# Optimization experiments

Measured on AMD Instinct MI355X. Metric: run time of the kernel, lower is better.

Reference implementation:

```python
import jax, jax.numpy as jnp
import numpy as np
from jax import lax

GUARD_CELLS = 80
BG_CELLS = 80
ALPHA = 1.8
CFAR_UNITS = 1 + 2 * GUARD_CELLS + 2 * BG_CELLS          # 321
GUARD_UNITS = 2 * GUARD_CELLS + 1                         # 161
BG_AREA = CFAR_UNITS ** 2 - GUARD_UNITS ** 2              # background ring cell count
FRONT_DIV = (GUARD_UNITS ** 2) * ALPHA


def box_sum(x, k):
    """Same-padded KxK box sum over NCHW x (C=1), via separable 1D convs.

    Mathematically identical to a Conv2d with all-ones KxK kernel, zero bias,
    padding (k-1)//2 -- but O(N*K) instead of O(N*K^2).
    """
    p = (k - 1) // 2
    kh = jnp.ones((1, 1, k, 1), x.dtype)  # OIHW
    kw = jnp.ones((1, 1, 1, k), x.dtype)
    y = lax.conv_general_dilated(x, kh, window_strides=(1, 1), padding=[(p, p), (0, 0)])
    y = lax.conv_general_dilated(y, kw, window_strides=(1, 1), padding=[(0, 0), (p, p)])
    return y


def setup_inputs() -> dict:
    key = jax.random.key(0)
    x = jax.random.uniform(key, (4, 1, 1024, 1024), dtype=jnp.float32)
    return {"x": x}


def reference(x) -> jnp.ndarray:
    allsum = box_sum(x, CFAR_UNITS)            # conv1: 321x321 ones box
    front = box_sum(x, GUARD_UNITS)            # conv2: 161x161 ones box
    back = (allsum - front) / jnp.float32(BG_AREA)     # div1: 1x1 conv = scale
    front = front / jnp.float32(FRONT_DIV)             # div2: 1x1 conv = scale
    return front / back
```

## Files before the change

### kernel.cpp

```cpp
#include <hip/hip_runtime.h>
#include <hip/hip_bf16.h>


#define IMG 4
#define H 1024
#define W 1024
#define NSEG 32
#define SEGR 32
#define PADL 164
#define PADR 164
#define ROWLEN (PADL + W + PADR)

__global__ __launch_bounds__(256) void hbox_kernel(const float* __restrict__ x,
                                                   float* __restrict__ h161,
                                                   float* __restrict__ h321) {
    __shared__ float P[4][ROWLEN];
    const int wave = threadIdx.x >> 6;
    const int lane = threadIdx.x & 63;
    const int row  = (blockIdx.x << 2) + wave;

    const float4* xr = reinterpret_cast<const float4*>(x + (size_t)row * W);
    float v[16];
    {
        float4 a0 = xr[(lane << 2) + 0];
        float4 a1 = xr[(lane << 2) + 1];
        float4 a2 = xr[(lane << 2) + 2];
        float4 a3 = xr[(lane << 2) + 3];
        v[0]=a0.x; v[1]=a0.y; v[2]=a0.z; v[3]=a0.w;
        v[4]=a1.x; v[5]=a1.y; v[6]=a1.z; v[7]=a1.w;
        v[8]=a2.x; v[9]=a2.y; v[10]=a2.z; v[11]=a2.w;
        v[12]=a3.x; v[13]=a3.y; v[14]=a3.z; v[15]=a3.w;
    }
    float s = 0.f;
#pragma unroll
    for (int j = 0; j < 16; ++j) { s += v[j]; v[j] = s; }
    float t = s;
#pragma unroll
    for (int d = 1; d < 64; d <<= 1) {
        float u = __shfl_up(t, d, 64);
        if (lane >= d) t += u;
    }
    const float off = t - s;
#pragma unroll
    for (int j = 0; j < 16; ++j) v[j] += off;
    const float tot = __shfl(t, 63, 64);

    float* rowP = P[wave];
    float4* Pr = reinterpret_cast<float4*>(rowP + PADL);
    Pr[(lane << 2) + 0] = make_float4(v[0], v[1], v[2], v[3]);
    Pr[(lane << 2) + 1] = make_float4(v[4], v[5], v[6], v[7]);
    Pr[(lane << 2) + 2] = make_float4(v[8], v[9], v[10], v[11]);
    Pr[(lane << 2) + 3] = make_float4(v[12], v[13], v[14], v[15]);
    {
        float4* Pz = reinterpret_cast<float4*>(rowP);
        if (lane < 41) {
            Pz[lane]       = make_float4(0.f, 0.f, 0.f, 0.f);
            Pz[297 + lane] = make_float4(tot, tot, tot, tot);
        }
    }
    __syncthreads();

    const float* Pw = &P[wave][PADL];
    float* o161 = h161 + (size_t)row * W;
    float* o321 = h321 + (size_t)row * W;
#pragma unroll
    for (int k = 0; k < 16; ++k) {
        const int c = lane + (k << 6);
        const float s1 = Pw[c + 80]  - Pw[c - 81];
        const float s3 = Pw[c + 160] - Pw[c - 161];
        o161[c] = s1;
        o321[c] = s3;
    }
}

__global__ __launch_bounds__(256) void vscan_kernel(float* __restrict__ h161,
                                                    float* __restrict__ h321,
                                                    float* __restrict__ Btot) {
    const int img = blockIdx.x >> 5;
    const int seg = blockIdx.x & 31;
    const int q   = threadIdx.x;
    const int r0  = seg << 5;

    float* buf = blockIdx.y ? h321 : h161;
    float4* p = reinterpret_cast<float4*>(buf + ((size_t)img << 20) + ((size_t)r0 << 10)) + q;

    float ax = 0.f, ay = 0.f, az = 0.f, aw = 0.f;
#pragma unroll
    for (int jj = 0; jj < SEGR; jj += 8) {
        float4 a[8];
#pragma unroll
        for (int j = 0; j < 8; ++j) a[j] = p[(size_t)(jj + j) << 8];
#pragma unroll
        for (int j = 0; j < 8; ++j) {
            ax += a[j].x; ay += a[j].y; az += a[j].z; aw += a[j].w;
            a[j] = make_float4(ax, ay, az, aw);
        }
#pragma unroll
        for (int j = 0; j < 8; ++j) p[(size_t)(jj + j) << 8] = a[j];
    }
    float4* bt = reinterpret_cast<float4*>(
        Btot + ((((size_t)blockIdx.y << 2) + img) << 15) + ((size_t)seg << 10));
    bt[q] = make_float4(ax, ay, az, aw);
}

__global__ __launch_bounds__(256) void segscan_kernel(const float* __restrict__ Btot,
                                                      float* __restrict__ SP) {
    const int wid    = (blockIdx.x << 2) + (threadIdx.x >> 6);
    const int lane   = threadIdx.x & 63;
    const int bufimg = wid >> 9;
    const int pairk  = wid & 511;
    const int col    = (pairk << 1) + (lane >> 5);
    const int segl   = lane & 31;

    const size_t idx = ((size_t)bufimg << 15) + ((size_t)segl << 10) + col;
    const float v = Btot[idx];
    float t = v;
#pragma unroll
    for (int d = 1; d < 32; d <<= 1) {
        const float u = __shfl_up(t, d, 64);
        if ((lane & 31) >= d) t += u;
    }
    SP[idx] = t - v;
}

__global__ __launch_bounds__(512) void final_kernel(const float* __restrict__ g161,
                                                    const float* __restrict__ g321,
                                                    const float* __restrict__ SP,
                                                    float* __restrict__ out) {
    const int img = blockIdx.x >> 9;
    const int r   = ((blockIdx.x & 511) << 1) + (threadIdx.x >> 8);
    const int c4  = threadIdx.x & 255;

    const float4* P1 = reinterpret_cast<const float4*>(g161 + ((size_t)img << 20));
    const float4* P3 = reinterpret_cast<const float4*>(g321 + ((size_t)img << 20));
    const float4* SP1 = reinterpret_cast<const float4*>(SP) + ((size_t)img << 13);
    const float4* SP3 = reinterpret_cast<const float4*>(SP) + ((size_t)(IMG + img) << 13);

    const int hi1 = min(r + 80, H - 1),  lo1 = r - 81;
    const int hi3 = min(r + 160, H - 1), lo3 = r - 161;

    float4 f  = P1[((size_t)hi1 << 8) + c4];
    float4 fs = SP1[(((size_t)hi1 >> 5) << 8) + c4];
    float fx = f.x + fs.x, fy = f.y + fs.y, fz = f.z + fs.z, fw = f.w + fs.w;
    if (lo1 >= 0) {
        float4 g  = P1[((size_t)lo1 << 8) + c4];
        float4 gs = SP1[(((size_t)lo1 >> 5) << 8) + c4];
        fx -= g.x + gs.x; fy -= g.y + gs.y; fz -= g.z + gs.z; fw -= g.w + gs.w;
    }
    float4 a  = P3[((size_t)hi3 << 8) + c4];
    float4 as = SP3[(((size_t)hi3 >> 5) << 8) + c4];
    float ax = a.x + as.x, ay = a.y + as.y, az = a.z + as.z, aw = a.w + as.w;
    if (lo3 >= 0) {
        float4 g  = P3[((size_t)lo3 << 8) + c4];
        float4 gs = SP3[(((size_t)lo3 >> 5) << 8) + c4];
        ax -= g.x + gs.x; ay -= g.y + gs.y; az -= g.z + gs.z; aw -= g.w + gs.w;
    }

    const float SCALE = (float)(77120.0 / 46657.8);
    float4 o;
    o.x = SCALE * fx * __builtin_amdgcn_rcpf(ax - fx);
    o.y = SCALE * fy * __builtin_amdgcn_rcpf(ay - fy);
    o.z = SCALE * fz * __builtin_amdgcn_rcpf(az - fz);
    o.w = SCALE * fw * __builtin_amdgcn_rcpf(aw - fw);
    reinterpret_cast<float4*>(out + ((size_t)img << 20) + ((size_t)r << 10))[c4] = o;
}

extern "C" void kernel_launch(void* const* d_in, const int* in_sizes, int n_in,
                              void* d_out, int out_size, void* d_ws, size_t ws_size,
                              hipStream_t stream) {
    const float* x = (const float*)d_in[0];
    float* outp = (float*)d_out;
    float* h161 = (float*)d_ws;
    float* h321 = h161 + (size_t)IMG * H * W;
    float* Btot = h321 + (size_t)IMG * H * W;
    float* SPb  = Btot + (size_t)2 * IMG * NSEG * W;

    hbox_kernel<<<dim3((IMG * H) / 4), dim3(256), 0, stream>>>(x, h161, h321);
    vscan_kernel<<<dim3(128, 2), dim3(256), 0, stream>>>(h161, h321, Btot);
    segscan_kernel<<<dim3(1024), dim3(256), 0, stream>>>(Btot, SPb);
    final_kernel<<<dim3(IMG * (H / 2)), dim3(512), 0, stream>>>(h161, h321, SPb, outp);
}
```

Before: 96.03 us.

## Fuse horizontal box sum with segmented vertical scan in one kernel

Merges the horizontal box-sum kernel and the vertical segment-scan kernel. Each block now takes 8 rows, computes the horizontal 161/321 sums through shared memory, and writes vertical prefix sums within 8-row segments directly. This removes the global read-modify-write pass over both intermediate buffers. The segment count grows to 128, so the segment-scan kernel now scans 128 totals per column. It also adds extra __syncthreads per block and a larger scan-offset array.

```diff
diff --git a/kernel.cpp b/kernel.cpp
--- a/kernel.cpp
+++ b/kernel.cpp
@@ -5,122 +5,137 @@
 #define IMG 4
 #define H 1024
 #define W 1024
-#define NSEG 32
-#define SEGR 32
+#define SEGR 8
+#define NSEG 128
 #define PADL 164
 #define PADR 164
 #define ROWLEN (PADL + W + PADR)
 
-__global__ __launch_bounds__(256) void hbox_kernel(const float* __restrict__ x,
-                                                   float* __restrict__ h161,
-                                                   float* __restrict__ h321) {
+__global__ __launch_bounds__(256, 4) void hbv_kernel(const float* __restrict__ x,
+                                                     float* __restrict__ g161,
+                                                     float* __restrict__ g321,
+                                                     float* __restrict__ Btot) {
     __shared__ float P[4][ROWLEN];
+    __shared__ float Hx[4][W];
     const int wave = threadIdx.x >> 6;
     const int lane = threadIdx.x & 63;
-    const int row  = (blockIdx.x << 2) + wave;
+    const int q    = threadIdx.x;
+    const int blk  = blockIdx.x;
+    const size_t rowbase = (size_t)blk << 3;
 
-    const float4* xr = reinterpret_cast<const float4*>(x + (size_t)row * W);
-    float v[16];
-    {
-        float4 a0 = xr[(lane << 2) + 0];
-        float4 a1 = xr[(lane << 2) + 1];
-        float4 a2 = xr[(lane << 2) + 2];
-        float4 a3 = xr[(lane << 2) + 3];
-        v[0]=a0.x; v[1]=a0.y; v[2]=a0.z; v[3]=a0.w;
-        v[4]=a1.x; v[5]=a1.y; v[6]=a1.z; v[7]=a1.w;
-        v[8]=a2.x; v[9]=a2.y; v[10]=a2.z; v[11]=a2.w;
-        v[12]=a3.x; v[13]=a3.y; v[14]=a3.z; v[15]=a3.w;
+    float4 acc1 = make_float4(0.f, 0.f, 0.f, 0.f);
+    float4 acc3 = make_float4(0.f, 0.f, 0.f, 0.f);
+
+#pragma unroll
+    for (int ch = 0; ch < 2; ++ch) {
+        const size_t row = rowbase + (ch << 2) + wave;
+        {
+            const float4* xr = reinterpret_cast<const float4*>(x + row * W);
+            float v[16];
+            float4 a0 = xr[(lane << 2) + 0];
+            float4 a1 = xr[(lane << 2) + 1];
+            float4 a2 = xr[(lane << 2) + 2];
+            float4 a3 = xr[(lane << 2) + 3];
+            v[0]=a0.x; v[1]=a0.y; v[2]=a0.z; v[3]=a0.w;
+            v[4]=a1.x; v[5]=a1.y; v[6]=a1.z; v[7]=a1.w;
+            v[8]=a2.x; v[9]=a2.y; v[10]=a2.z; v[11]=a2.w;
+            v[12]=a3.x; v[13]=a3.y; v[14]=a3.z; v[15]=a3.w;
+            float s = 0.f;
+#pragma unroll
+            for (int j = 0; j < 16; ++j) { s += v[j]; v[j] = s; }
+            float t = s;
+#pragma unroll
+            for (int d = 1; d < 64; d <<= 1) {
+                float u = __shfl_up(t, d, 64);
+                if (lane >= d) t += u;
+            }
+            const float off = t - s;
+#pragma unroll
+            for (int j = 0; j < 16; ++j) v[j] += off;
+            const float tot = __shfl(t, 63, 64);
+
+            float* rowP = P[wave];
+            float4* Pr = reinterpret_cast<float4*>(rowP + PADL);
+            Pr[(lane << 2) + 0] = make_float4(v[0], v[1], v[2], v[3]);
+            Pr[(lane << 2) + 1] = make_float4(v[4], v[5], v[6], v[7]);
+            Pr[(lane << 2) + 2] = make_float4(v[8], v[9], v[10], v[11]);
+            Pr[(lane << 2) + 3] = make_float4(v[12], v[13], v[14], v[15]);
+            float4* Pz = reinterpret_cast<float4*>(rowP);
+            if (lane < 41) {
+                Pz[lane]       = make_float4(0.f, 0.f, 0.f, 0.f);
+                Pz[297 + lane] = make_float4(tot, tot, tot, tot);
+            }
+        }
+        const float* Pw = &P[wave][PADL];
+
+#pragma unroll
+        for (int k = 0; k < 16; ++k) {
+            const int c = lane + (k << 6);
+            Hx[wave][c] = Pw[c + 80] - Pw[c - 81];
+        }
+        __syncthreads();
+        {
+            float* o = g161 + (rowbase + (ch << 2)) * W;
+            const float4* Hf = reinterpret_cast<const float4*>(Hx);
+#pragma unroll
+            for (int r = 0; r < 4; ++r) {
+                float4 h = Hf[(r << 8) + q];
+                acc1.x += h.x; acc1.y += h.y; acc1.z += h.z; acc1.w += h.w;
+                reinterpret_cast<float4*>(o + (size_t)r * W)[q] = acc1;
+            }
+        }
+        __syncthreads();
+#pragma unroll
+        for (int k = 0; k < 16; ++k) {
+            const int c = lane + (k << 6);
+            Hx[wave][c] = Pw[c + 160] - Pw[c - 161];
+        }
+        __syncthreads();
+        {
+            float* o = g321 + (rowbase + (ch << 2)) * W;
+            const float4* Hf = reinterpret_cast<const float4*>(Hx);
+#pragma unroll
+            for (int r = 0; r < 4; ++r) {
+                float4 h = Hf[(r << 8) + q];
+                acc3.x += h.x; acc3.y += h.y; acc3.z += h.z; acc3.w += h.w;
+                reinterpret_cast<float4*>(o + (size_t)r * W)[q] = acc3;
+            }
+        }
+        __syncthreads();
     }
-    float s = 0.f;
-#pragma unroll
-    for (int j = 0; j < 16; ++j) { s += v[j]; v[j] = s; }
-    float t = s;
-#pragma unroll
-    for (int d = 1; d < 64; d <<= 1) {
-        float u = __shfl_up(t, d, 64);
-        if (lane >= d) t += u;
-    }
-    const float off = t - s;
-#pragma unroll
-    for (int j = 0; j < 16; ++j) v[j] += off;
-    const float tot = __shfl(t, 63, 64);
 
-    float* rowP = P[wave];
-    float4* Pr = reinterpret_cast<float4*>(rowP + PADL);
-    Pr[(lane << 2) + 0] = make_float4(v[0], v[1], v[2], v[3]);
-    Pr[(lane << 2) + 1] = make_float4(v[4], v[5], v[6], v[7]);
-    Pr[(lane << 2) + 2] = make_float4(v[8], v[9], v[10], v[11]);
-    Pr[(lane << 2) + 3] = make_float4(v[12], v[13], v[14], v[15]);
-    {
-        float4* Pz = reinterpret_cast<float4*>(rowP);
-        if (lane < 41) {
-            Pz[lane]       = make_float4(0.f, 0.f, 0.f, 0.f);
-            Pz[297 + lane] = make_float4(tot, tot, tot, tot);
-        }
-    }
-    __syncthreads();
-
-    const float* Pw = &P[wave][PADL];
-    float* o161 = h161 + (size_t)row * W;
-    float* o321 = h321 + (size_t)row * W;
-#pragma unroll
-    for (int k = 0; k < 16; ++k) {
-        const int c = lane + (k << 6);
-        const float s1 = Pw[c + 80]  - Pw[c - 81];
-        const float s3 = Pw[c + 160] - Pw[c - 161];
-        o161[c] = s1;
-        o321[c] = s3;
-    }
-}
-
-__global__ __launch_bounds__(256) void vscan_kernel(float* __restrict__ h161,
-                                                    float* __restrict__ h321,
-                                                    float* __restrict__ Btot) {
-    const int img = blockIdx.x >> 5;
-    const int seg = blockIdx.x & 31;
-    const int q   = threadIdx.x;
-    const int r0  = seg << 5;
-
-    float* buf = blockIdx.y ? h321 : h161;
-    float4* p = reinterpret_cast<float4*>(buf + ((size_t)img << 20) + ((size_t)r0 << 10)) + q;
-
-    float ax = 0.f, ay = 0.f, az = 0.f, aw = 0.f;
-#pragma unroll
-    for (int jj = 0; jj < SEGR; jj += 8) {
-        float4 a[8];
-#pragma unroll
-        for (int j = 0; j < 8; ++j) a[j] = p[(size_t)(jj + j) << 8];
-#pragma unroll
-        for (int j = 0; j < 8; ++j) {
-            ax += a[j].x; ay += a[j].y; az += a[j].z; aw += a[j].w;
-            a[j] = make_float4(ax, ay, az, aw);
-        }
-#pragma unroll
-        for (int j = 0; j < 8; ++j) p[(size_t)(jj + j) << 8] = a[j];
-    }
-    float4* bt = reinterpret_cast<float4*>(
-        Btot + ((((size_t)blockIdx.y << 2) + img) << 15) + ((size_t)seg << 10));
-    bt[q] = make_float4(ax, ay, az, aw);
+    const int img = blk >> 7;
+    const int seg = blk & 127;
+    float4* bt = reinterpret_cast<float4*>(Btot);
+    bt[((size_t)img << 15)         + (seg << 8) + q] = acc1;
+    bt[((size_t)(IMG + img) << 15) + (seg << 8) + q] = acc3;
 }
 
 __global__ __launch_bounds__(256) void segscan_kernel(const float* __restrict__ Btot,
                                                       float* __restrict__ SP) {
-    const int wid    = (blockIdx.x << 2) + (threadIdx.x >> 6);
-    const int lane   = threadIdx.x & 63;
-    const int bufimg = wid >> 9;
-    const int pairk  = wid & 511;
-    const int col    = (pairk << 1) + (lane >> 5);
-    const int segl   = lane & 31;
+    const int wid  = (blockIdx.x << 2) + (threadIdx.x >> 6);
+    const int lane = threadIdx.x & 63;
+    const int bi   = wid >> 10;
+    const int col  = wid & 1023;
+    const size_t base = ((size_t)bi << 17) + col;
 
-    const size_t idx = ((size_t)bufimg << 15) + ((size_t)segl << 10) + col;
-    const float v = Btot[idx];
-    float t = v;
+    const float a = Btot[base + ((size_t)lane << 10)];
+    const float b = Btot[base + ((size_t)(64 + lane) << 10)];
+    float t = a;
 #pragma unroll
-    for (int d = 1; d < 32; d <<= 1) {
+    for (int d = 1; d < 64; d <<= 1) {
         const float u = __shfl_up(t, d, 64);
-        if ((lane & 31) >= d) t += u;
+        if (lane >= d) t += u;
     }
-    SP[idx] = t - v;
+    const float T = __shfl(t, 63, 64);
+    float s = b;
+#pragma unroll
+    for (int d = 1; d < 64; d <<= 1) {
+        const float u = __shfl_up(s, d, 64);
+        if (lane >= d) s += u;
+    }
+    SP[base + ((size_t)lane << 10)]        = t - a;
+    SP[base + ((size_t)(64 + lane) << 10)] = T + s - b;
 }
 
 __global__ __launch_bounds__(512) void final_kernel(const float* __restrict__ g161,
@@ -133,26 +148,26 @@
 
     const float4* P1 = reinterpret_cast<const float4*>(g161 + ((size_t)img << 20));
     const float4* P3 = reinterpret_cast<const float4*>(g321 + ((size_t)img << 20));
-    const float4* SP1 = reinterpret_cast<const float4*>(SP) + ((size_t)img << 13);
-    const float4* SP3 = reinterpret_cast<const float4*>(SP) + ((size_t)(IMG + img) << 13);
+    const float4* SP1 = reinterpret_cast<const float4*>(SP) + ((size_t)img << 15);
+    const float4* SP3 = reinterpret_cast<const float4*>(SP) + ((size_t)(IMG + img) << 15);
 
     const int hi1 = min(r + 80, H - 1),  lo1 = r - 81;
     const int hi3 = min(r + 160, H - 1), lo3 = r - 161;
 
     float4 f  = P1[((size_t)hi1 << 8) + c4];
-    float4 fs = SP1[(((size_t)hi1 >> 5) << 8) + c4];
+    float4 fs = SP1[(((size_t)hi1 >> 3) << 8) + c4];
     float fx = f.x + fs.x, fy = f.y + fs.y, fz = f.z + fs.z, fw = f.w + fs.w;
     if (lo1 >= 0) {
         float4 g  = P1[((size_t)lo1 << 8) + c4];
-        float4 gs = SP1[(((size_t)lo1 >> 5) << 8) + c4];
+        float4 gs = SP1[(((size_t)lo1 >> 3) << 8) + c4];
         fx -= g.x + gs.x; fy -= g.y + gs.y; fz -= g.z + gs.z; fw -= g.w + gs.w;
     }
     float4 a  = P3[((size_t)hi3 << 8) + c4];
-    float4 as = SP3[(((size_t)hi3 >> 5) << 8) + c4];
+    float4 as = SP3[(((size_t)hi3 >> 3) << 8) + c4];
     float ax = a.x + as.x, ay = a.y + as.y, az = a.z + as.z, aw = a.w + as.w;
     if (lo3 >= 0) {
         float4 g  = P3[((size_t)lo3 << 8) + c4];
-        float4 gs = SP3[(((size_t)lo3 >> 5) << 8) + c4];
+        float4 gs = SP3[(((size_t)lo3 >> 3) << 8) + c4];
         ax -= g.x + gs.x; ay -= g.y + gs.y; az -= g.z + gs.z; aw -= g.w + gs.w;
     }
 
@@ -170,13 +185,12 @@
                               hipStream_t stream) {
     const float* x = (const float*)d_in[0];
     float* outp = (float*)d_out;
-    float* h161 = (float*)d_ws;
-    float* h321 = h161 + (size_t)IMG * H * W;
-    float* Btot = h321 + (size_t)IMG * H * W;
+    float* g161 = (float*)d_ws;
+    float* g321 = g161 + (size_t)IMG * H * W;
+    float* Btot = g321 + (size_t)IMG * H * W;
     float* SPb  = Btot + (size_t)2 * IMG * NSEG * W;
 
-    hbox_kernel<<<dim3((IMG * H) / 4), dim3(256), 0, stream>>>(x, h161, h321);
-    vscan_kernel<<<dim3(128, 2), dim3(256), 0, stream>>>(h161, h321, Btot);
-    segscan_kernel<<<dim3(1024), dim3(256), 0, stream>>>(Btot, SPb);
-    final_kernel<<<dim3(IMG * (H / 2)), dim3(512), 0, stream>>>(h161, h321, SPb, outp);
+    hbv_kernel<<<dim3(IMG * NSEG), dim3(256), 0, stream>>>(x, g161, g321, Btot);
+    segscan_kernel<<<dim3(2048), dim3(256), 0, stream>>>(Btot, SPb);
+    final_kernel<<<dim3(IMG * (H / 2)), dim3(512), 0, stream>>>(g161, g321, SPb, outp);
 }
```

After: 99.60 us. 1.04x slower.

## Fuse vertical scan, segment scan and final pass into one cooperative kernel

Applied to the files above, without the earlier changes.

Merges the three post-horizontal kernels into a single cooperative launch of 1024 blocks that uses grid-wide syncs between the per-segment vertical scan, the cross-segment scan and the final ratio pass. Segments shrink from 32 rows to 8, giving 4x more blocks in the scan phase for parallelism, and the segment prefix scan becomes a 128-wide wave scan. This removes two kernel launch boundaries. In exchange it pays for grid barriers, depends on all 1024 blocks being co-resident, and enlarges the segment-total and prefix buffers in the workspace.

```diff
diff --git a/kernel.cpp b/kernel.cpp
--- a/kernel.cpp
+++ b/kernel.cpp
@@ -1,12 +1,15 @@
 #include <hip/hip_runtime.h>
 #include <hip/hip_bf16.h>
+#include <hip/hip_cooperative_groups.h>
+
+namespace cg = cooperative_groups;
 
 
 #define IMG 4
 #define H 1024
 #define W 1024
-#define NSEG 32
-#define SEGR 32
+#define SEGR 8
+#define NSEG 128
 #define PADL 164
 #define PADR 164
 #define ROWLEN (PADL + W + PADR)
@@ -73,96 +76,106 @@
     }
 }
 
-__global__ __launch_bounds__(256) void vscan_kernel(float* __restrict__ h161,
-                                                    float* __restrict__ h321,
-                                                    float* __restrict__ Btot) {
-    const int img = blockIdx.x >> 5;
-    const int seg = blockIdx.x & 31;
-    const int q   = threadIdx.x;
-    const int r0  = seg << 5;
+__global__ __launch_bounds__(256, 4) void vsf_kernel(float* __restrict__ g161,
+                                                     float* __restrict__ g321,
+                                                     float* __restrict__ Btot,
+                                                     float* __restrict__ SP,
+                                                     float* __restrict__ out) {
+    cg::grid_group grid = cg::this_grid();
+    const int tid = threadIdx.x;
+    const int bid = blockIdx.x;
 
-    float* buf = blockIdx.y ? h321 : h161;
-    float4* p = reinterpret_cast<float4*>(buf + ((size_t)img << 20) + ((size_t)r0 << 10)) + q;
-
-    float ax = 0.f, ay = 0.f, az = 0.f, aw = 0.f;
+    {
+        const int buf = bid >> 9;
+        const int img = (bid >> 7) & 3;
+        const int seg = bid & 127;
+        float* b = buf ? g321 : g161;
+        float4* p = reinterpret_cast<float4*>(
+            b + ((size_t)img << 20) + ((size_t)(seg << 3) << 10)) + tid;
+        float4 a[SEGR];
 #pragma unroll
-    for (int jj = 0; jj < SEGR; jj += 8) {
-        float4 a[8];
+        for (int j = 0; j < SEGR; ++j) a[j] = p[(size_t)j << 8];
 #pragma unroll
-        for (int j = 0; j < 8; ++j) a[j] = p[(size_t)(jj + j) << 8];
-#pragma unroll
-        for (int j = 0; j < 8; ++j) {
-            ax += a[j].x; ay += a[j].y; az += a[j].z; aw += a[j].w;
-            a[j] = make_float4(ax, ay, az, aw);
+        for (int j = 1; j < SEGR; ++j) {
+            a[j].x += a[j-1].x; a[j].y += a[j-1].y;
+            a[j].z += a[j-1].z; a[j].w += a[j-1].w;
         }
 #pragma unroll
-        for (int j = 0; j < 8; ++j) p[(size_t)(jj + j) << 8] = a[j];
+        for (int j = 1; j < SEGR; ++j) p[(size_t)j << 8] = a[j];
+        float4* bt = reinterpret_cast<float4*>(
+            Btot + (((size_t)(buf << 2) + img) << 17) + ((size_t)seg << 10));
+        bt[tid] = a[SEGR - 1];
     }
-    float4* bt = reinterpret_cast<float4*>(
-        Btot + ((((size_t)blockIdx.y << 2) + img) << 15) + ((size_t)seg << 10));
-    bt[q] = make_float4(ax, ay, az, aw);
-}
+    grid.sync();
 
-__global__ __launch_bounds__(256) void segscan_kernel(const float* __restrict__ Btot,
-                                                      float* __restrict__ SP) {
-    const int wid    = (blockIdx.x << 2) + (threadIdx.x >> 6);
-    const int lane   = threadIdx.x & 63;
-    const int bufimg = wid >> 9;
-    const int pairk  = wid & 511;
-    const int col    = (pairk << 1) + (lane >> 5);
-    const int segl   = lane & 31;
+    {
+        const int wv   = (bid << 2) + (tid >> 6);
+        const int lane = tid & 63;
+#pragma unroll
+        for (int k = 0; k < 2; ++k) {
+            const int cu  = wv + (k << 12);
+            const int bi  = cu >> 10;
+            const int col = cu & 1023;
+            const float* bt = Btot + ((size_t)bi << 17) + col;
+            float*       sp = SP   + ((size_t)bi << 17) + col;
+            const float v0 = bt[(size_t)(lane << 1) << 10];
+            const float v1 = bt[(size_t)((lane << 1) + 1) << 10];
+            const float s  = v0 + v1;
+            float t = s;
+#pragma unroll
+            for (int d = 1; d < 64; d <<= 1) {
+                const float u = __shfl_up(t, d, 64);
+                if (lane >= d) t += u;
+            }
+            const float e = t - s;
+            sp[(size_t)(lane << 1) << 10]       = e;
+            sp[(size_t)((lane << 1) + 1) << 10] = e + v0;
+        }
+    }
+    grid.sync();
 
-    const size_t idx = ((size_t)bufimg << 15) + ((size_t)segl << 10) + col;
-    const float v = Btot[idx];
-    float t = v;
+    {
+        const float SCALE = (float)(77120.0 / 46657.8);
+        const int c4 = tid;
 #pragma unroll
-    for (int d = 1; d < 32; d <<= 1) {
-        const float u = __shfl_up(t, d, 64);
-        if ((lane & 31) >= d) t += u;
+        for (int rr = 0; rr < 4; ++rr) {
+            const int fr  = (bid << 2) + rr;
+            const int img = fr >> 10;
+            const int r   = fr & 1023;
+
+            const float4* P1 = reinterpret_cast<const float4*>(g161 + ((size_t)img << 20));
+            const float4* P3 = reinterpret_cast<const float4*>(g321 + ((size_t)img << 20));
+            const float4* SP1 = reinterpret_cast<const float4*>(SP) + ((size_t)img << 15);
+            const float4* SP3 = reinterpret_cast<const float4*>(SP) + ((size_t)(IMG + img) << 15);
+
+            const int hi1 = min(r + 80, H - 1),  lo1 = r - 81;
+            const int hi3 = min(r + 160, H - 1), lo3 = r - 161;
+
+            float4 f  = P1[((size_t)hi1 << 8) + c4];
+            float4 fs = SP1[(((size_t)hi1 >> 3) << 8) + c4];
+            float fx = f.x + fs.x, fy = f.y + fs.y, fz = f.z + fs.z, fw = f.w + fs.w;
+            if (lo1 >= 0) {
+                float4 g  = P1[((size_t)lo1 << 8) + c4];
+                float4 gs = SP1[(((size_t)lo1 >> 3) << 8) + c4];
+                fx -= g.x + gs.x; fy -= g.y + gs.y; fz -= g.z + gs.z; fw -= g.w + gs.w;
+            }
+            float4 a  = P3[((size_t)hi3 << 8) + c4];
+            float4 as = SP3[(((size_t)hi3 >> 3) << 8) + c4];
+            float ax = a.x + as.x, ay = a.y + as.y, az = a.z + as.z, aw = a.w + as.w;
+            if (lo3 >= 0) {
+                float4 g  = P3[((size_t)lo3 << 8) + c4];
+                float4 gs = SP3[(((size_t)lo3 >> 3) << 8) + c4];
+                ax -= g.x + gs.x; ay -= g.y + gs.y; az -= g.z + gs.z; aw -= g.w + gs.w;
+            }
+
+            float4 o;
+            o.x = SCALE * fx * __builtin_amdgcn_rcpf(ax - fx);
+            o.y = SCALE * fy * __builtin_amdgcn_rcpf(ay - fy);
+            o.z = SCALE * fz * __builtin_amdgcn_rcpf(az - fz);
+            o.w = SCALE * fw * __builtin_amdgcn_rcpf(aw - fw);
+            reinterpret_cast<float4*>(out + ((size_t)img << 20) + ((size_t)r << 10))[c4] = o;
+        }
     }
-    SP[idx] = t - v;
-}
-
-__global__ __launch_bounds__(512) void final_kernel(const float* __restrict__ g161,
-                                                    const float* __restrict__ g321,
-                                                    const float* __restrict__ SP,
-                                                    float* __restrict__ out) {
-    const int img = blockIdx.x >> 9;
-    const int r   = ((blockIdx.x & 511) << 1) + (threadIdx.x >> 8);
-    const int c4  = threadIdx.x & 255;
-
-    const float4* P1 = reinterpret_cast<const float4*>(g161 + ((size_t)img << 20));
-    const float4* P3 = reinterpret_cast<const float4*>(g321 + ((size_t)img << 20));
-    const float4* SP1 = reinterpret_cast<const float4*>(SP) + ((size_t)img << 13);
-    const float4* SP3 = reinterpret_cast<const float4*>(SP) + ((size_t)(IMG + img) << 13);
-
-    const int hi1 = min(r + 80, H - 1),  lo1 = r - 81;
-    const int hi3 = min(r + 160, H - 1), lo3 = r - 161;
-
-    float4 f  = P1[((size_t)hi1 << 8) + c4];
-    float4 fs = SP1[(((size_t)hi1 >> 5) << 8) + c4];
-    float fx = f.x + fs.x, fy = f.y + fs.y, fz = f.z + fs.z, fw = f.w + fs.w;
-    if (lo1 >= 0) {
-        float4 g  = P1[((size_t)lo1 << 8) + c4];
-        float4 gs = SP1[(((size_t)lo1 >> 5) << 8) + c4];
-        fx -= g.x + gs.x; fy -= g.y + gs.y; fz -= g.z + gs.z; fw -= g.w + gs.w;
-    }
-    float4 a  = P3[((size_t)hi3 << 8) + c4];
-    float4 as = SP3[(((size_t)hi3 >> 5) << 8) + c4];
-    float ax = a.x + as.x, ay = a.y + as.y, az = a.z + as.z, aw = a.w + as.w;
-    if (lo3 >= 0) {
-        float4 g  = P3[((size_t)lo3 << 8) + c4];
-        float4 gs = SP3[(((size_t)lo3 >> 5) << 8) + c4];
-        ax -= g.x + gs.x; ay -= g.y + gs.y; az -= g.z + gs.z; aw -= g.w + gs.w;
-    }
-
-    const float SCALE = (float)(77120.0 / 46657.8);
-    float4 o;
-    o.x = SCALE * fx * __builtin_amdgcn_rcpf(ax - fx);
-    o.y = SCALE * fy * __builtin_amdgcn_rcpf(ay - fy);
-    o.z = SCALE * fz * __builtin_amdgcn_rcpf(az - fz);
-    o.w = SCALE * fw * __builtin_amdgcn_rcpf(aw - fw);
-    reinterpret_cast<float4*>(out + ((size_t)img << 20) + ((size_t)r << 10))[c4] = o;
 }
 
 extern "C" void kernel_launch(void* const* d_in, const int* in_sizes, int n_in,
@@ -170,13 +183,14 @@
                               hipStream_t stream) {
     const float* x = (const float*)d_in[0];
     float* outp = (float*)d_out;
-    float* h161 = (float*)d_ws;
-    float* h321 = h161 + (size_t)IMG * H * W;
-    float* Btot = h321 + (size_t)IMG * H * W;
+    float* g161 = (float*)d_ws;
+    float* g321 = g161 + (size_t)IMG * H * W;
+    float* Btot = g321 + (size_t)IMG * H * W;
     float* SPb  = Btot + (size_t)2 * IMG * NSEG * W;
 
-    hbox_kernel<<<dim3((IMG * H) / 4), dim3(256), 0, stream>>>(x, h161, h321);
-    vscan_kernel<<<dim3(128, 2), dim3(256), 0, stream>>>(h161, h321, Btot);
-    segscan_kernel<<<dim3(1024), dim3(256), 0, stream>>>(Btot, SPb);
-    final_kernel<<<dim3(IMG * (H / 2)), dim3(512), 0, stream>>>(h161, h321, SPb, outp);
+    hbox_kernel<<<dim3((IMG * H) / 4), dim3(256), 0, stream>>>(x, g161, g321);
+
+    void* args[] = {&g161, &g321, &Btot, &SPb, &outp};
+    hipLaunchCooperativeKernel((void*)vsf_kernel, dim3(IMG * NSEG * 2),
+                               dim3(256), args, 0, stream);
 }
```

New measurement: 345.8 us. +260.1%, slower.
